# Performance work log

Hardware: AMD Instinct MI355X
Metric: run time of the kernel (lower is better)

## Reference

```python
import jax, jax.numpy as jnp
import numpy as np

WS = 16        # window size
NH = 8         # num heads
EPS = 1e-6
BN_EPS = 1e-5


def _l2norm(t):
    # normalize along the channel (d) axis, which is axis=-2, per position
    return t / jnp.linalg.norm(t, axis=-2, keepdims=True)


def setup_inputs() -> dict:
    key = jax.random.key(0)
    k1, k2, k3 = jax.random.split(key, 3)
    B, C, H, W = 8, 96, 256, 256
    x = jax.random.normal(k1, (B, C, H, W), dtype=jnp.float32)
    w_qkv = jax.random.normal(k2, (3 * C, C), dtype=jnp.float32) * (1.0 / np.sqrt(C))
    w_proj = jax.random.normal(k3, (C, C), dtype=jnp.float32) * (1.0 / np.sqrt(C))
    gamma = jnp.ones((C,), dtype=jnp.float32)
    beta = jnp.zeros((C,), dtype=jnp.float32)
    return {"x": x, "w_qkv": w_qkv, "w_proj": w_proj, "gamma": gamma, "beta": beta}


def reference(x, w_qkv, w_proj, gamma, beta):
    B, C, H, W = x.shape
    ws, nh = WS, NH
    d = C // nh
    # pad H, W up to multiples of ws (static shapes -> jit-safe)
    Hp = (H + ws - 1) // ws * ws
    Wp = (W + ws - 1) // ws * ws
    if (Hp, Wp) != (H, W):
        x = jnp.pad(x, ((0, 0), (0, 0), (0, Hp - H), (0, Wp - W)))
    hh, ww = Hp // ws, Wp // ws

    # 1x1 conv qkv projection (no bias)
    qkv = jnp.einsum('oc,bchw->bohw', w_qkv, x)  # [B, 3C, Hp, Wp]
    # rearrange 'b (qkv h d) (hh ws1) (ww ws2) -> qkv (b hh ww) h d (ws1 ws2)'
    qkv = qkv.reshape(B, 3, nh, d, hh, ws, ww, ws)
    qkv = qkv.transpose(1, 0, 4, 6, 2, 3, 5, 7).reshape(3, B * hh * ww, nh, d, ws * ws)
    q, k, v = qkv[0], qkv[1], qkv[2]  # each [bw, h, d, n]  (n = ws*ws)

    q = _l2norm(q).transpose(0, 1, 3, 2)  # [bw, h, n, d]
    k = _l2norm(k)                        # [bw, h, d, n]

    ksum = k.sum(axis=-1) + EPS           # [bw, h, d]
    tailor = 1.0 / (ws * ws + jnp.einsum('bhnc,bhc->bhn', q, ksum))  # [bw, h, n]

    kv = jnp.einsum('bhmn,bhcn->bhmc', k, v)     # [bw, h, d, d]
    attn = jnp.einsum('bhnm,bhmc->bhcn', q, kv)  # [bw, h, d, n]
    attn = attn + v.sum(axis=-1, keepdims=True)  # broadcast sum_n v over n
    attn = attn * tailor[:, :, None, :]

    # rearrange '(b hh ww) h d (ws1 ws2) -> b (h d) (hh ws1) (ww ws2)'
    out = attn.reshape(B, hh, ww, nh, d, ws, ws)
    out = out.transpose(0, 3, 4, 1, 5, 2, 6).reshape(B, C, Hp, Wp)
    out = out[:, :, :H, :W]

    # proj: 1x1 conv + BatchNorm2d (training-mode batch statistics)
    y = jnp.einsum('oc,bchw->bohw', w_proj, out)
    mean = y.mean(axis=(0, 2, 3), keepdims=True)
    var = y.var(axis=(0, 2, 3), keepdims=True)
    y = (y - mean) * jax.lax.rsqrt(var + BN_EPS)
    y = y * gamma[None, :, None, None] + beta[None, :, None, None]
    return y
```

## Files before the change

kernel.cpp:

```cpp
#include <hip/hip_runtime.h>

typedef short s8v __attribute__((ext_vector_type(8)));
typedef float f4v __attribute__((ext_vector_type(4)));

union F8 { int4 i; s8v s; };

__device__ __forceinline__ short f2bf(float f){
  union {float f; unsigned u;} v; v.f = f;
  unsigned r = (v.u + 0x7FFFu + ((v.u >> 16) & 1u)) >> 16;
  return (short)r;
}

#define MFMA(a,b,c) __builtin_amdgcn_mfma_f32_16x16x32_bf16((a),(b),(c),0,0,0)

#define WS_W2_OFF   58368
#define WS_ST_OFF   76800
#define WS_OUT_OFF  (1u<<20)

__global__ void prep_kernel(const float* __restrict__ wqkv, const float* __restrict__ wproj,
                            unsigned short* __restrict__ w1, unsigned short* __restrict__ w2,
                            float* __restrict__ stats){
  int i = blockIdx.x * 256 + threadIdx.x;
  for (int j = i; j < 304*96; j += gridDim.x * 256){
    int row = j / 96, c = j - row * 96;
    float v = (row < 288) ? wqkv[row * 96 + c] : 0.f;
    w1[j] = (unsigned short)f2bf(v);
  }
  for (int j = i; j < 96*96; j += gridDim.x * 256)
    w2[j] = (unsigned short)f2bf(wproj[j]);
  if (i < 192) stats[i] = 0.f;
}

__global__ __launch_bounds__(256) void attn_kernel(const float* __restrict__ x,
                                                   const unsigned short* __restrict__ w1,
                                                   short* __restrict__ outp){
  __shared__ short ks[2][16*264];
  __shared__ short vs[2][16*264];
  __shared__ short qsT[256*40];

  const int tid  = threadIdx.x;
  const int lane = tid & 63, wave = tid >> 6;
  const int quad = lane >> 4, col = lane & 15;
  const int wx = blockIdx.x, wy = blockIdx.y, b = blockIdx.z;
  const int h0 = wy * 16, w0 = wx * 16;

  for (int i = tid; i < 2*4*264; i += 256){
    int buf = i / (4*264), j = i % (4*264);
    int r = 12 + j / 264, cc = j % 264;
    short v = (r == 15) ? (short)0x3F80 : (short)0;
    ks[buf][r*264 + cc] = v; vs[buf][r*264 + cc] = v;
  }
  for (int i = tid; i < 256*40; i += 256)
    qsT[i] = ((i % 40) == 12) ? (short)0x3F80 : (short)0;

  const float* xb = x + ((size_t)b * 96 << 16);
  s8v Bf[4][3];
  #pragma unroll
  for (int jt = 0; jt < 4; ++jt){
    int t0 = wave * 64 + jt * 16;
    const float* px = xb + (size_t)(h0 + (t0 >> 4)) * 256 + (w0 + col);
    #pragma unroll
    for (int kt = 0; kt < 3; ++kt){
      F8 f;
      #pragma unroll
      for (int j = 0; j < 8; ++j){
        int c = kt * 32 + quad * 8 + j;
        f.s[j] = f2bf(px[(size_t)c << 16]);
      }
      Bf[jt][kt] = f.s;
    }
  }

  for (int h = 0; h < 8; ++h){
    const int p = h & 1;
    {
      s8v Aq[3];
      #pragma unroll
      for (int kt = 0; kt < 3; ++kt){
        F8 f; f.i = *(const int4*)(w1 + (h*12 + col) * 96 + kt*32 + quad*8);
        Aq[kt] = f.s;
      }
      #pragma unroll
      for (int jt = 0; jt < 4; ++jt){
        f4v a = {0.f,0.f,0.f,0.f};
        #pragma unroll
        for (int kt = 0; kt < 3; ++kt) a = MFMA(Aq[kt], Bf[jt][kt], a);
        float s = (quad < 3) ? (a[0]*a[0] + a[1]*a[1] + a[2]*a[2] + a[3]*a[3]) : 0.f;
        s += __shfl_xor(s, 16, 64); s += __shfl_xor(s, 32, 64);
        float rq = rsqrtf(s);
        if (quad < 3){
          int t = wave*64 + jt*16 + col;
          short4 pk; pk.x = f2bf(a[0]*rq); pk.y = f2bf(a[1]*rq); pk.z = f2bf(a[2]*rq); pk.w = f2bf(a[3]*rq);
          *(short4*)&qsT[t*40 + quad*4] = pk;
        }
      }
    }
    {
      s8v Ak[3];
      #pragma unroll
      for (int kt = 0; kt < 3; ++kt){
        F8 f; f.i = *(const int4*)(w1 + (96 + h*12 + col) * 96 + kt*32 + quad*8);
        Ak[kt] = f.s;
      }
      #pragma unroll
      for (int jt = 0; jt < 4; ++jt){
        f4v a = {0.f,0.f,0.f,0.f};
        #pragma unroll
        for (int kt = 0; kt < 3; ++kt) a = MFMA(Ak[kt], Bf[jt][kt], a);
        float s = (quad < 3) ? (a[0]*a[0] + a[1]*a[1] + a[2]*a[2] + a[3]*a[3]) : 0.f;
        s += __shfl_xor(s, 16, 64); s += __shfl_xor(s, 32, 64);
        float rk = rsqrtf(s);
        if (quad < 3){
          int t = wave*64 + jt*16 + col;
          #pragma unroll
          for (int r = 0; r < 4; ++r) ks[p][(quad*4 + r)*264 + t] = f2bf(a[r]*rk);
        }
      }
    }
    {
      s8v Av[3];
      #pragma unroll
      for (int kt = 0; kt < 3; ++kt){
        F8 f; f.i = *(const int4*)(w1 + (192 + h*12 + col) * 96 + kt*32 + quad*8);
        Av[kt] = f.s;
      }
      #pragma unroll
      for (int jt = 0; jt < 4; ++jt){
        f4v a = {0.f,0.f,0.f,0.f};
        #pragma unroll
        for (int kt = 0; kt < 3; ++kt) a = MFMA(Av[kt], Bf[jt][kt], a);
        if (quad < 3){
          int t = wave*64 + jt*16 + col;
          #pragma unroll
          for (int r = 0; r < 4; ++r) vs[p][(quad*4 + r)*264 + t] = f2bf(a[r]);
        }
      }
    }
    __syncthreads();

    f4v kvv = {0.f,0.f,0.f,0.f};
    #pragma unroll
    for (int kk = 0; kk < 8; ++kk){
      F8 a, bv;
      a.i  = *(const int4*)&ks[p][col*264 + kk*32 + quad*8];
      bv.i = *(const int4*)&vs[p][col*264 + kk*32 + quad*8];
      kvv = MFMA(a.s, bv.s, kvv);
    }
    F8 fa;
    {
      int cc = (col == 12) ? 15 : col;
      int l0 = ((quad << 1) << 4) | cc;
      int l1 = (((quad << 1) + 1) << 4) | cc;
      float v;
      v = __shfl(kvv[0], l0 & 63, 64); fa.s[0] = f2bf((quad < 2) ? v : 0.f);
      v = __shfl(kvv[1], l0 & 63, 64); fa.s[1] = f2bf((quad < 2) ? v : 0.f);
      v = __shfl(kvv[2], l0 & 63, 64); fa.s[2] = f2bf((quad < 2) ? v : 0.f);
      v = __shfl(kvv[3], l0 & 63, 64); fa.s[3] = f2bf((quad < 2) ? v : 0.f);
      float v0  = __shfl(kvv[0], l1 & 63, 64);
      float v15 = __shfl(kvv[3], 48 | cc, 64);
      fa.s[4] = f2bf((quad == 0) ? v0 : ((quad == 1) ? v15 : 0.f));
      v = __shfl(kvv[1], l1 & 63, 64); fa.s[5] = f2bf((quad == 0) ? v : 0.f);
      v = __shfl(kvv[2], l1 & 63, 64); fa.s[6] = f2bf((quad == 0) ? v : 0.f);
      v = __shfl(kvv[3], l1 & 63, 64); fa.s[7] = f2bf((quad == 0) ? v : 0.f);
    }
    #pragma unroll
    for (int jt = 0; jt < 4; ++jt){
      int t0 = wave*64 + jt*16;
      F8 bq; bq.i = *(const int4*)&qsT[(t0 + col)*40 + quad*8];
      f4v z = {0.f,0.f,0.f,0.f};
      f4v d2 = MFMA(fa.s, bq.s, z);
      float dot = __shfl(d2[0], 48 + col, 64);
      float tl = 1.f / dot;
      if (quad < 3){
        int pix = (h0 + (t0 >> 4)) * 256 + (w0 + col);
        short* po = outp + ((size_t)(b << 16) + pix) * 96 + h*12 + quad*4;
        short4 pk; pk.x = f2bf(d2[0]*tl); pk.y = f2bf(d2[1]*tl); pk.z = f2bf(d2[2]*tl); pk.w = f2bf(d2[3]*tl);
        *(short4*)po = pk;
      }
    }
  }
}

__global__ __launch_bounds__(256) void proj_kernel(const short* __restrict__ outp,
                                                   const unsigned short* __restrict__ w2,
                                                   float* __restrict__ y,
                                                   float* __restrict__ stats){
  __shared__ float sld[192];
  const int tid = threadIdx.x;
  if (tid < 192) sld[tid] = 0.f;
  __syncthreads();
  const int lane = tid & 63, wave = tid >> 6;
  const int quad = lane >> 4, col = lane & 15;
  const int hrow = blockIdx.x, b = blockIdx.y;

  const size_t pixbase = (size_t)(b << 16) + (size_t)hrow * 256;
  s8v Bf[4][3];
  #pragma unroll
  for (int jt = 0; jt < 4; ++jt){
    int n0 = wave*64 + jt*16;
    const short* pb = outp + (pixbase + n0 + col) * 96 + quad*8;
    #pragma unroll
    for (int kt = 0; kt < 3; ++kt){
      F8 f; f.i = *(const int4*)(pb + kt*32);
      Bf[jt][kt] = f.s;
    }
  }
  float* yb = y + ((size_t)(b*96) << 16) + (size_t)hrow * 256;
  #pragma unroll
  for (int mt = 0; mt < 6; ++mt){
    s8v Af[3];
    #pragma unroll
    for (int kt = 0; kt < 3; ++kt){
      F8 f; f.i = *(const int4*)(w2 + (mt*16 + col)*96 + kt*32 + quad*8);
      Af[kt] = f.s;
    }
    float rs[4] = {0.f,0.f,0.f,0.f}, rss[4] = {0.f,0.f,0.f,0.f};
    #pragma unroll
    for (int jt = 0; jt < 4; ++jt){
      int n0 = wave*64 + jt*16;
      f4v a = {0.f,0.f,0.f,0.f};
      #pragma unroll
      for (int kt = 0; kt < 3; ++kt) a = MFMA(Af[kt], Bf[jt][kt], a);
      float* pyo = yb + ((size_t)(mt*16 + quad*4) << 16) + n0 + col;
      #pragma unroll
      for (int r = 0; r < 4; ++r){
        float v = a[r];
        pyo[(size_t)r << 16] = v;
        rs[r] += v; rss[r] += v * v;
      }
    }
    #pragma unroll
    for (int r = 0; r < 4; ++r){
      float a1 = rs[r], a2 = rss[r];
      a1 += __shfl_xor(a1, 1, 64); a2 += __shfl_xor(a2, 1, 64);
      a1 += __shfl_xor(a1, 2, 64); a2 += __shfl_xor(a2, 2, 64);
      a1 += __shfl_xor(a1, 4, 64); a2 += __shfl_xor(a2, 4, 64);
      a1 += __shfl_xor(a1, 8, 64); a2 += __shfl_xor(a2, 8, 64);
      if (col == 0){
        int o = mt*16 + quad*4 + r;
        atomicAdd(&sld[o], a1);
        atomicAdd(&sld[96 + o], a2);
      }
    }
  }
  __syncthreads();
  if (tid < 192) atomicAdd(&stats[tid], sld[tid]);
}

__global__ __launch_bounds__(256) void bn_kernel(float* __restrict__ y,
                                                 const float* __restrict__ stats,
                                                 const float* __restrict__ gamma,
                                                 const float* __restrict__ beta){
  const int qq = blockIdx.x, c = blockIdx.y, b = blockIdx.z;
  const float invN = 1.f / 524288.f;
  float s = stats[c], ss = stats[96 + c];
  float mean = s * invN;
  float var  = ss * invN - mean * mean;
  float sc = gamma[c] * rsqrtf(var + 1e-5f);
  float sh = beta[c] - mean * sc;
  float4* p = (float4*)(y + ((size_t)(b * 96 + c) << 16) + (size_t)qq * 16384);
  int tid = threadIdx.x;
  #pragma unroll
  for (int i = 0; i < 16; ++i){
    float4 v = p[tid + i * 256];
    v.x = v.x * sc + sh; v.y = v.y * sc + sh; v.z = v.z * sc + sh; v.w = v.w * sc + sh;
    p[tid + i * 256] = v;
  }
}

extern "C" void kernel_launch(void* const* d_in, const int* in_sizes, int n_in,
                              void* d_out, int out_size, void* d_ws, size_t ws_size,
                              hipStream_t stream){
  const float* x     = (const float*)d_in[0];
  const float* wqkv  = (const float*)d_in[1];
  const float* wproj = (const float*)d_in[2];
  const float* gamma = (const float*)d_in[3];
  const float* beta  = (const float*)d_in[4];
  char* ws = (char*)d_ws;
  unsigned short* w1 = (unsigned short*)(ws);
  unsigned short* w2 = (unsigned short*)(ws + WS_W2_OFF);
  float* stats = (float*)(ws + WS_ST_OFF);
  short* outp  = (short*)(ws + WS_OUT_OFF);
  float* y = (float*)d_out;

  hipLaunchKernelGGL(prep_kernel, dim3(64), dim3(256), 0, stream, wqkv, wproj, w1, w2, stats);
  hipLaunchKernelGGL(attn_kernel, dim3(16, 16, 8), dim3(256), 0, stream, x, w1, outp);
  hipLaunchKernelGGL(proj_kernel, dim3(256, 8), dim3(256), 0, stream, outp, w2, y, stats);
  hipLaunchKernelGGL(bn_kernel, dim3(4, 96, 8), dim3(256), 0, stream, y, stats, gamma, beta);
}
```

Measured before the change: 606.9 us.

## Recompute projection for batchnorm instead of storing and rereading pre-norm output

The projection now runs twice. One pass only accumulates the batch statistics, and a second pass recomputes the projection and applies the normalization before writing y once. This removes the separate full write plus read-modify-write of the large fp32 output, at the cost of reading the bf16 intermediate twice and redoing the MFMAs. The attention kernel also builds the q fragment in registers through shuffles instead of an LDS round-trip. Its output layout changes to head-major with 12 channels per head, and the projection weight is padded to 128 columns to match. Launch bounds now request higher occupancy.

```diff
diff --git a/kernel.cpp b/kernel.cpp
--- a/kernel.cpp
+++ b/kernel.cpp
@@ -4,6 +4,7 @@
 typedef float f4v __attribute__((ext_vector_type(4)));
 
 union F8 { int4 i; s8v s; };
+union F8L { long long l[2]; s8v s; };
 
 __device__ __forceinline__ short f2bf(float f){
   union {float f; unsigned u;} v; v.f = f;
@@ -14,11 +15,11 @@
 #define MFMA(a,b,c) __builtin_amdgcn_mfma_f32_16x16x32_bf16((a),(b),(c),0,0,0)
 
 #define WS_W2_OFF   58368
-#define WS_ST_OFF   76800
+#define WS_ST_OFF   82944
 #define WS_OUT_OFF  (1u<<20)
 
 __global__ void prep_kernel(const float* __restrict__ wqkv, const float* __restrict__ wproj,
-                            unsigned short* __restrict__ w1, unsigned short* __restrict__ w2,
+                            unsigned short* __restrict__ w1, unsigned short* __restrict__ w2p,
                             float* __restrict__ stats){
   int i = blockIdx.x * 256 + threadIdx.x;
   for (int j = i; j < 304*96; j += gridDim.x * 256){
@@ -26,17 +27,19 @@
     float v = (row < 288) ? wqkv[row * 96 + c] : 0.f;
     w1[j] = (unsigned short)f2bf(v);
   }
-  for (int j = i; j < 96*96; j += gridDim.x * 256)
-    w2[j] = (unsigned short)f2bf(wproj[j]);
+  for (int j = i; j < 96*128; j += gridDim.x * 256){
+    int o = j >> 7, c = j & 127, h = c >> 4, ii = c & 15;
+    float v = (ii < 12) ? wproj[o * 96 + h * 12 + ii] : 0.f;
+    w2p[j] = (unsigned short)f2bf(v);
+  }
   if (i < 192) stats[i] = 0.f;
 }
 
-__global__ __launch_bounds__(256) void attn_kernel(const float* __restrict__ x,
-                                                   const unsigned short* __restrict__ w1,
-                                                   short* __restrict__ outp){
+__global__ __launch_bounds__(256,4) void attn_kernel(const float* __restrict__ x,
+                                                     const unsigned short* __restrict__ w1,
+                                                     short* __restrict__ outp){
   __shared__ short ks[2][16*264];
   __shared__ short vs[2][16*264];
-  __shared__ short qsT[256*40];
 
   const int tid  = threadIdx.x;
   const int lane = tid & 63, wave = tid >> 6;
@@ -50,8 +53,6 @@
     short v = (r == 15) ? (short)0x3F80 : (short)0;
     ks[buf][r*264 + cc] = v; vs[buf][r*264 + cc] = v;
   }
-  for (int i = tid; i < 256*40; i += 256)
-    qsT[i] = ((i % 40) == 12) ? (short)0x3F80 : (short)0;
 
   const float* xb = x + ((size_t)b * 96 << 16);
   s8v Bf[4][3];
@@ -73,6 +74,7 @@
 
   for (int h = 0; h < 8; ++h){
     const int p = h & 1;
+    s8v bq[4];
     {
       s8v Aq[3];
       #pragma unroll
@@ -88,11 +90,24 @@
         float s = (quad < 3) ? (a[0]*a[0] + a[1]*a[1] + a[2]*a[2] + a[3]*a[3]) : 0.f;
         s += __shfl_xor(s, 16, 64); s += __shfl_xor(s, 32, 64);
         float rq = rsqrtf(s);
-        if (quad < 3){
-          int t = wave*64 + jt*16 + col;
-          short4 pk; pk.x = f2bf(a[0]*rq); pk.y = f2bf(a[1]*rq); pk.z = f2bf(a[2]*rq); pk.w = f2bf(a[3]*rq);
-          *(short4*)&qsT[t*40 + quad*4] = pk;
-        }
+        float q0 = a[0]*rq, q1 = a[1]*rq, q2 = a[2]*rq, q3 = a[3]*rq;
+        int s0 = (quad == 0) ? col        : (32 + col);
+        int s1 = (quad == 0) ? (16 + col) : (32 + col);
+        float v0 = __shfl(q0, s0, 64), v1 = __shfl(q1, s0, 64);
+        float v2 = __shfl(q2, s0, 64), v3 = __shfl(q3, s0, 64);
+        float w4 = __shfl(q0, s1, 64), w5 = __shfl(q1, s1, 64);
+        float w6 = __shfl(q2, s1, 64), w7 = __shfl(q3, s1, 64);
+        F8 f;
+        bool lo = (quad < 2);
+        f.s[0] = lo ? f2bf(v0) : (short)0;
+        f.s[1] = lo ? f2bf(v1) : (short)0;
+        f.s[2] = lo ? f2bf(v2) : (short)0;
+        f.s[3] = lo ? f2bf(v3) : (short)0;
+        f.s[4] = (quad == 0) ? f2bf(w4) : ((quad == 1) ? (short)0x3F80 : (short)0);
+        f.s[5] = (quad == 0) ? f2bf(w5) : (short)0;
+        f.s[6] = (quad == 0) ? f2bf(w6) : (short)0;
+        f.s[7] = (quad == 0) ? f2bf(w7) : (short)0;
+        bq[jt] = f.s;
       }
     }
     {
@@ -166,14 +181,13 @@
     #pragma unroll
     for (int jt = 0; jt < 4; ++jt){
       int t0 = wave*64 + jt*16;
-      F8 bq; bq.i = *(const int4*)&qsT[(t0 + col)*40 + quad*8];
       f4v z = {0.f,0.f,0.f,0.f};
-      f4v d2 = MFMA(fa.s, bq.s, z);
+      f4v d2 = MFMA(fa.s, bq[jt], z);
       float dot = __shfl(d2[0], 48 + col, 64);
       float tl = 1.f / dot;
       if (quad < 3){
         int pix = (h0 + (t0 >> 4)) * 256 + (w0 + col);
-        short* po = outp + ((size_t)(b << 16) + pix) * 96 + h*12 + quad*4;
+        short* po = outp + ((size_t)((b*8 + h) * 65536 + pix)) * 12 + quad*4;
         short4 pk; pk.x = f2bf(d2[0]*tl); pk.y = f2bf(d2[1]*tl); pk.z = f2bf(d2[2]*tl); pk.w = f2bf(d2[3]*tl);
         *(short4*)po = pk;
       }
@@ -181,10 +195,27 @@
   }
 }
 
-__global__ __launch_bounds__(256) void proj_kernel(const short* __restrict__ outp,
-                                                   const unsigned short* __restrict__ w2,
-                                                   float* __restrict__ y,
-                                                   float* __restrict__ stats){
+__device__ __forceinline__ void load_proj_bfrag(const short* __restrict__ outp,
+                                                int b, int pixrow, int wave, int quad, int col,
+                                                s8v Bf[4][4]){
+  #pragma unroll
+  for (int jt = 0; jt < 4; ++jt){
+    int pix = pixrow + wave*64 + jt*16 + col;
+    #pragma unroll
+    for (int kt = 0; kt < 4; ++kt){
+      int h = kt*2 + (quad >> 1);
+      const short* pb = outp + ((size_t)((b*8 + h) * 65536 + pix)) * 12;
+      F8L f;
+      if ((quad & 1) == 0){ f.l[0] = *(const long long*)(pb);     f.l[1] = *(const long long*)(pb + 4); }
+      else                { f.l[0] = *(const long long*)(pb + 8); f.l[1] = 0; }
+      Bf[jt][kt] = f.s;
+    }
+  }
+}
+
+__global__ __launch_bounds__(256,4) void projstats_kernel(const short* __restrict__ outp,
+                                                          const unsigned short* __restrict__ w2p,
+                                                          float* __restrict__ stats){
   __shared__ float sld[192];
   const int tid = threadIdx.x;
   if (tid < 192) sld[tid] = 0.f;
@@ -193,41 +224,25 @@
   const int quad = lane >> 4, col = lane & 15;
   const int hrow = blockIdx.x, b = blockIdx.y;
 
-  const size_t pixbase = (size_t)(b << 16) + (size_t)hrow * 256;
-  s8v Bf[4][3];
-  #pragma unroll
-  for (int jt = 0; jt < 4; ++jt){
-    int n0 = wave*64 + jt*16;
-    const short* pb = outp + (pixbase + n0 + col) * 96 + quad*8;
-    #pragma unroll
-    for (int kt = 0; kt < 3; ++kt){
-      F8 f; f.i = *(const int4*)(pb + kt*32);
-      Bf[jt][kt] = f.s;
-    }
-  }
-  float* yb = y + ((size_t)(b*96) << 16) + (size_t)hrow * 256;
+  s8v Bf[4][4];
+  load_proj_bfrag(outp, b, hrow*256, wave, quad, col, Bf);
+
   #pragma unroll
   for (int mt = 0; mt < 6; ++mt){
-    s8v Af[3];
-    #pragma unroll
-    for (int kt = 0; kt < 3; ++kt){
-      F8 f; f.i = *(const int4*)(w2 + (mt*16 + col)*96 + kt*32 + quad*8);
+    s8v Af[4];
+    #pragma unroll
+    for (int kt = 0; kt < 4; ++kt){
+      F8 f; f.i = *(const int4*)(w2p + (mt*16 + col)*128 + kt*32 + quad*8);
       Af[kt] = f.s;
     }
     float rs[4] = {0.f,0.f,0.f,0.f}, rss[4] = {0.f,0.f,0.f,0.f};
     #pragma unroll
     for (int jt = 0; jt < 4; ++jt){
-      int n0 = wave*64 + jt*16;
       f4v a = {0.f,0.f,0.f,0.f};
       #pragma unroll
-      for (int kt = 0; kt < 3; ++kt) a = MFMA(Af[kt], Bf[jt][kt], a);
-      float* pyo = yb + ((size_t)(mt*16 + quad*4) << 16) + n0 + col;
-      #pragma unroll
-      for (int r = 0; r < 4; ++r){
-        float v = a[r];
-        pyo[(size_t)r << 16] = v;
-        rs[r] += v; rss[r] += v * v;
-      }
+      for (int kt = 0; kt < 4; ++kt) a = MFMA(Af[kt], Bf[jt][kt], a);
+      #pragma unroll
+      for (int r = 0; r < 4; ++r){ float v = a[r]; rs[r] += v; rss[r] += v*v; }
     }
     #pragma unroll
     for (int r = 0; r < 4; ++r){
@@ -247,24 +262,50 @@
   if (tid < 192) atomicAdd(&stats[tid], sld[tid]);
 }
 
-__global__ __launch_bounds__(256) void bn_kernel(float* __restrict__ y,
-                                                 const float* __restrict__ stats,
-                                                 const float* __restrict__ gamma,
-                                                 const float* __restrict__ beta){
-  const int qq = blockIdx.x, c = blockIdx.y, b = blockIdx.z;
-  const float invN = 1.f / 524288.f;
-  float s = stats[c], ss = stats[96 + c];
-  float mean = s * invN;
-  float var  = ss * invN - mean * mean;
-  float sc = gamma[c] * rsqrtf(var + 1e-5f);
-  float sh = beta[c] - mean * sc;
-  float4* p = (float4*)(y + ((size_t)(b * 96 + c) << 16) + (size_t)qq * 16384);
-  int tid = threadIdx.x;
+__global__ __launch_bounds__(256,4) void projbn_kernel(const short* __restrict__ outp,
+                                                       const unsigned short* __restrict__ w2p,
+                                                       const float* __restrict__ stats,
+                                                       const float* __restrict__ gamma,
+                                                       const float* __restrict__ beta,
+                                                       float* __restrict__ y){
+  __shared__ float sc[96], sh[96];
+  const int tid = threadIdx.x;
+  if (tid < 96){
+    const float invN = 1.f / 524288.f;
+    float m  = stats[tid] * invN;
+    float var = stats[96 + tid] * invN - m*m;
+    float s = gamma[tid] * rsqrtf(var + 1e-5f);
+    sc[tid] = s; sh[tid] = beta[tid] - m * s;
+  }
+  __syncthreads();
+  const int lane = tid & 63, wave = tid >> 6;
+  const int quad = lane >> 4, col = lane & 15;
+  const int hrow = blockIdx.x, b = blockIdx.y;
+
+  s8v Bf[4][4];
+  load_proj_bfrag(outp, b, hrow*256, wave, quad, col, Bf);
+
+  float* yb = y + ((size_t)(b*96) << 16) + (size_t)hrow * 256;
   #pragma unroll
-  for (int i = 0; i < 16; ++i){
-    float4 v = p[tid + i * 256];
-    v.x = v.x * sc + sh; v.y = v.y * sc + sh; v.z = v.z * sc + sh; v.w = v.w * sc + sh;
-    p[tid + i * 256] = v;
+  for (int mt = 0; mt < 6; ++mt){
+    s8v Af[4];
+    #pragma unroll
+    for (int kt = 0; kt < 4; ++kt){
+      F8 f; f.i = *(const int4*)(w2p + (mt*16 + col)*128 + kt*32 + quad*8);
+      Af[kt] = f.s;
+    }
+    #pragma unroll
+    for (int jt = 0; jt < 4; ++jt){
+      int n0 = wave*64 + jt*16;
+      f4v a = {0.f,0.f,0.f,0.f};
+      #pragma unroll
+      for (int kt = 0; kt < 4; ++kt) a = MFMA(Af[kt], Bf[jt][kt], a);
+      #pragma unroll
+      for (int r = 0; r < 4; ++r){
+        int ch = mt*16 + quad*4 + r;
+        yb[((size_t)ch << 16) + n0 + col] = a[r] * sc[ch] + sh[ch];
+      }
+    }
   }
 }
 
@@ -277,14 +318,14 @@
   const float* gamma = (const float*)d_in[3];
   const float* beta  = (const float*)d_in[4];
   char* ws = (char*)d_ws;
-  unsigned short* w1 = (unsigned short*)(ws);
-  unsigned short* w2 = (unsigned short*)(ws + WS_W2_OFF);
+  unsigned short* w1  = (unsigned short*)(ws);
+  unsigned short* w2p = (unsigned short*)(ws + WS_W2_OFF);
   float* stats = (float*)(ws + WS_ST_OFF);
   short* outp  = (short*)(ws + WS_OUT_OFF);
   float* y = (float*)d_out;
 
-  hipLaunchKernelGGL(prep_kernel, dim3(64), dim3(256), 0, stream, wqkv, wproj, w1, w2, stats);
+  hipLaunchKernelGGL(prep_kernel, dim3(64), dim3(256), 0, stream, wqkv, wproj, w1, w2p, stats);
   hipLaunchKernelGGL(attn_kernel, dim3(16, 16, 8), dim3(256), 0, stream, x, w1, outp);
-  hipLaunchKernelGGL(proj_kernel, dim3(256, 8), dim3(256), 0, stream, outp, w2, y, stats);
-  hipLaunchKernelGGL(bn_kernel, dim3(4, 96, 8), dim3(256), 0, stream, y, stats, gamma, beta);
-}
+  hipLaunchKernelGGL(projstats_kernel, dim3(256, 8), dim3(256), 0, stream, outp, w2p, stats);
+  hipLaunchKernelGGL(projbn_kernel, dim3(256, 8), dim3(256), 0, stream, outp, w2p, stats, gamma, beta, y);
+}
```

Result: faster. 542.4 us (-10.6%).
